# Optimization experiments

Measured on AMD Instinct MI355X. Metric: run time of the kernel, lower is better.

Reference implementation:

```python
import jax, jax.numpy as jnp
import numpy as np

NUM_NODES = 100000
NUM_EDGES = 1600000
NUM_GRAPHS = 64
D_IN = 128
HID = 256
N_ATTR = 8
D_OUT = 1


def setup_inputs() -> dict:
    key = jax.random.key(0)
    ks = jax.random.split(key, 16)
    x = jax.random.normal(ks[0], (NUM_NODES, D_IN), dtype=jnp.float32)
    edge_index = jax.random.randint(ks[1], (2, NUM_EDGES), 0, NUM_NODES, dtype=jnp.int64)
    batch = jnp.sort(jax.random.randint(ks[2], (NUM_NODES,), 0, NUM_GRAPHS, dtype=jnp.int64))
    graph_attr = jax.random.normal(ks[3], (NUM_GRAPHS, N_ATTR), dtype=jnp.float32)
    def lin(k, fi, fo):
        s = 1.0 / np.sqrt(fi)
        return jax.random.uniform(k, (fi, fo), jnp.float32, -s, s)
    # SAGEConv: lin_l (applied to aggregated neighbors, has bias) + lin_r (root, no bias)
    W1l = lin(ks[4], D_IN, HID); b1 = jnp.zeros((HID,), jnp.float32)
    W1r = lin(ks[5], D_IN, HID)
    W2l = lin(ks[6], HID, HID); b2 = jnp.zeros((HID,), jnp.float32)
    W2r = lin(ks[7], HID, HID)
    Wf1 = lin(ks[8], HID + N_ATTR, HID); bf1 = jnp.zeros((HID,), jnp.float32)
    Wf2 = lin(ks[9], HID, D_OUT); bf2 = jnp.zeros((D_OUT,), jnp.float32)
    return {"x": x, "edge_index": edge_index, "batch": batch, "graph_attr": graph_attr,
            "W1l": W1l, "b1": b1, "W1r": W1r, "W2l": W2l, "b2": b2, "W2r": W2r,
            "Wf1": Wf1, "bf1": bf1, "Wf2": Wf2, "bf2": bf2}


def _mean_agg(h, src, dst, num_segments):
    # gather source features, scatter-mean into destination nodes
    s = jax.ops.segment_sum(h[src], dst, num_segments=num_segments)
    cnt = jax.ops.segment_sum(jnp.ones((src.shape[0], 1), h.dtype), dst, num_segments=num_segments)
    return s / jnp.maximum(cnt, 1.0)


def _sage(h, src, dst, Wl, b, Wr):
    agg = _mean_agg(h, src, dst, h.shape[0])
    return agg @ Wl + b + h @ Wr


def reference(x, edge_index, batch, graph_attr, W1l, b1, W1r, W2l, b2, W2r, Wf1, bf1, Wf2, bf2):
    src, dst = edge_index[0], edge_index[1]
    h = jax.nn.relu(_sage(x, src, dst, W1l, b1, W1r))
    h = _sage(h, src, dst, W2l, b2, W2r)
    # global mean pool over graphs
    gsum = jax.ops.segment_sum(h, batch, num_segments=NUM_GRAPHS)
    gcnt = jax.ops.segment_sum(jnp.ones((h.shape[0], 1), h.dtype), batch, num_segments=NUM_GRAPHS)
    g = gsum / jnp.maximum(gcnt, 1.0)
    g = jnp.concatenate([g, graph_attr.reshape(-1, N_ATTR)], axis=1)
    g = jax.nn.relu(g @ Wf1 + bf1)
    return g @ Wf2 + bf2
```

## Files before the change

### kernel.cpp

```cpp
#include <hip/hip_runtime.h>
#include <stdint.h>

#define NN 100000
#define NE 1600000
#define NG 64
#define DIN 128
#define HID 256
#define NATTR 8
#define NBK 391
#define CAP 6144
#define PCH 4096
#define BWW 25000
#define CB 12756

typedef unsigned short u16;
typedef __attribute__((ext_vector_type(8))) short s16x8;
typedef __attribute__((ext_vector_type(4))) float f32x4;

__device__ __forceinline__ int imaxi(int a, int b) { return a > b ? a : b; }
__device__ __forceinline__ u16 f2bf(float f) {
    unsigned u = __float_as_uint(f);
    return (u16)((u + 0x7fffu + ((u >> 16) & 1u)) >> 16);
}
__device__ __forceinline__ void gload16(const void* g, void* l) {
    __builtin_amdgcn_global_load_lds((const __attribute__((address_space(1))) void*)g,
                                     (__attribute__((address_space(3))) void*)l, 16, 0, 0);
}


__global__ void k_prep(const float4* __restrict__ x4, ushort4* __restrict__ xb4,
                       const float* __restrict__ W1l, const float* __restrict__ W1r,
                       u16* __restrict__ W1lt, u16* __restrict__ W1rt,
                       float4* __restrict__ P84, const int* __restrict__ batch,
                       int* __restrict__ goff, int* __restrict__ gcnt,
                       int* __restrict__ cursor) {
    int b = blockIdx.x, t = threadIdx.x;
    if (b < CB) {
        int i = b * 256 + t;
        const int NX4 = NN * DIN / 4;
        if (i < NX4) {
            float4 v = x4[i];
            ushort4 o;
            o.x = f2bf(v.x); o.y = f2bf(v.y); o.z = f2bf(v.z); o.w = f2bf(v.w);
            xb4[i] = o;
        } else {
            int j = i - NX4;
            if (j < 32768) {
                int n = j >> 7, k = j & 127;
                W1lt[j] = f2bf(W1l[k * HID + n]);
            } else if (j < 65536) {
                int jj = j - 32768;
                int n = jj >> 7, k = jj & 127;
                W1rt[jj] = f2bf(W1r[k * HID + n]);
            }
        }
    } else if (b < CB + 256) {
        int i = (b - CB) * 256 + t;
        P84[i] = make_float4(0.f, 0.f, 0.f, 0.f);
    } else {
        for (int i = t; i < NBK; i += 256) cursor[i] = 0;
        int g = t;
        if (g <= NG) {
            int lo = 0, hi = NN;
            while (lo < hi) {
                int mid = (lo + hi) >> 1;
                if (batch[mid] < g) lo = mid + 1; else hi = mid;
            }
            goff[g] = lo;
        }
        __syncthreads();
        if (g < NG) gcnt[g] = goff[g + 1] - goff[g];
    }
}


__global__ __launch_bounds__(256) void k_part(const int* __restrict__ ei,
                                              int* __restrict__ cursor,
                                              unsigned* __restrict__ pairs) {
    __shared__ unsigned spk[PCH];
    __shared__ unsigned short sbk[PCH];
    __shared__ int hist[NBK], gb[NBK];
    __shared__ int sc[512];
    int t = threadIdx.x;
    int c0 = blockIdx.x * PCH;
    int n = NE - c0; if (n > PCH) n = PCH;
    for (int i = t; i < NBK; i += 256) hist[i] = 0;
    __syncthreads();
    unsigned mypk[16]; unsigned short mybk[16]; int myoff[16];
#pragma unroll
    for (int j = 0; j < 16; j++) {
        int i = t + j * 256;
        myoff[j] = -1;
        if (i < n) {
            int e = c0 + i;
            unsigned d = (unsigned)__builtin_nontemporal_load(&ei[NE + e]);
            unsigned s = (unsigned)__builtin_nontemporal_load(&ei[e]);
            unsigned bk = d >> 8;
            mypk[j] = ((d & 255u) << 24) | s;
            mybk[j] = (unsigned short)bk;
            myoff[j] = atomicAdd(&hist[bk], 1);
        }
    }
    __syncthreads();
    sc[t] = (t < NBK) ? hist[t] : 0;
    sc[t + 256] = (t + 256 < NBK) ? hist[t + 256] : 0;
    __syncthreads();
    for (int off = 1; off < 512; off <<= 1) {
        int v0 = (t >= off) ? sc[t - off] : 0;
        int v1 = (t + 256 >= off) ? sc[t + 256 - off] : 0;
        __syncthreads();
        sc[t] += v0; sc[t + 256] += v1;
        __syncthreads();
    }
    if (t < NBK && hist[t] > 0) gb[t] = atomicAdd(&cursor[t], hist[t]);
    if (t + 256 < NBK && hist[t + 256] > 0)
        gb[t + 256] = atomicAdd(&cursor[t + 256], hist[t + 256]);
    __syncthreads();
#pragma unroll
    for (int j = 0; j < 16; j++) {
        if (myoff[j] >= 0) {
            int bk = mybk[j];
            int pos = sc[bk] - hist[bk] + myoff[j];
            spk[pos] = mypk[j];
            sbk[pos] = (unsigned short)bk;
        }
    }
    __syncthreads();
    for (int i = t; i < n; i += 256) {
        int bk = sbk[i];
        int local = gb[bk] + (i - (sc[bk] - hist[bk]));
        pairs[(size_t)bk * CAP + local] = spk[i];
    }
}


__global__ __launch_bounds__(256) void k_csr(const unsigned* __restrict__ pairs,
                                             const int* __restrict__ cursor,
                                             int* __restrict__ rowptr,
                                             unsigned* __restrict__ col) {
    __shared__ unsigned colL[CAP];
    __shared__ int csc[512];
    __shared__ int cnt[256], cur[256], sc[256];
    int b = blockIdx.x, t = threadIdx.x;
    csc[t] = (t < NBK) ? cursor[t] : 0;
    csc[t + 256] = (t + 256 < NBK) ? cursor[t + 256] : 0;
    __syncthreads();
    for (int off = 1; off < 512; off <<= 1) {
        int v0 = (t >= off) ? csc[t - off] : 0;
        int v1 = (t + 256 >= off) ? csc[t + 256 - off] : 0;
        __syncthreads();
        csc[t] += v0; csc[t + 256] += v1;
        __syncthreads();
    }
    int obase = (b == 0) ? 0 : csc[b - 1];
    int ecnt = cursor[b];
    const unsigned* pp = pairs + (size_t)b * CAP;
    cnt[t] = 0;
    __syncthreads();
    for (int i = t; i < ecnt; i += 256)
        atomicAdd(&cnt[pp[i] >> 24], 1);
    __syncthreads();
    sc[t] = cnt[t];
    __syncthreads();
    for (int off = 1; off < 256; off <<= 1) {
        int v = (t >= off) ? sc[t - off] : 0;
        __syncthreads();
        sc[t] += v;
        __syncthreads();
    }
    int lr = sc[t] - cnt[t];
    cur[t] = lr;
    int node = (b << 8) + t;
    if (node < NN) rowptr[node] = obase + lr;
    if (b == NBK - 1 && t == 0) rowptr[NN] = obase + ecnt;
    __syncthreads();
    for (int i = t; i < ecnt; i += 256) {
        unsigned p = pp[i];
        int dl = p >> 24;
        int pos = atomicAdd(&cur[dl], 1);
        int dd = cnt[dl]; if (dd > 32767) dd = 32767;
        colL[pos] = ((unsigned)dd << 17) | (p & 0xFFFFFFu);
    }
    __syncthreads();
    for (int i = t; i < ecnt; i += 256)
        col[obase + i] = colL[i];
}


__global__ void k_agg(const uint4* __restrict__ xb4, uint4* __restrict__ agg4,
                      const int* __restrict__ rowptr, const unsigned* __restrict__ col) {
    int node = blockIdx.x * 4 + (threadIdx.x >> 6);
    int lane = threadIdx.x & 63;
    if (node >= NN) return;
    int qtr = lane >> 4, li = lane & 15;
    int s = rowptr[node], e = rowptr[node + 1];
    float a0 = 0, a1 = 0, a2 = 0, a3 = 0, a4 = 0, a5 = 0, a6 = 0, a7 = 0;
#define ACC8(V) do { \
        a0 += __uint_as_float((V).x << 16); a1 += __uint_as_float((V).x & 0xffff0000u); \
        a2 += __uint_as_float((V).y << 16); a3 += __uint_as_float((V).y & 0xffff0000u); \
        a4 += __uint_as_float((V).z << 16); a5 += __uint_as_float((V).z & 0xffff0000u); \
        a6 += __uint_as_float((V).w << 16); a7 += __uint_as_float((V).w & 0xffff0000u); } while (0)
    int i = s;
    for (; i + 16 <= e; i += 16) {
        unsigned c0 = col[i + qtr] & 0x1FFFFu;
        unsigned c1 = col[i + 4 + qtr] & 0x1FFFFu;
        unsigned c2 = col[i + 8 + qtr] & 0x1FFFFu;
        unsigned c3 = col[i + 12 + qtr] & 0x1FFFFu;
        uint4 w0 = xb4[(size_t)c0 * 16 + li];
        uint4 w1 = xb4[(size_t)c1 * 16 + li];
        uint4 w2 = xb4[(size_t)c2 * 16 + li];
        uint4 w3 = xb4[(size_t)c3 * 16 + li];
        ACC8(w0); ACC8(w1); ACC8(w2); ACC8(w3);
    }
    for (; i + 4 <= e; i += 4) {
        unsigned c = col[i + qtr] & 0x1FFFFu;
        uint4 wv = xb4[(size_t)c * 16 + li];
        ACC8(wv);
    }
    if (i + qtr < e) {
        unsigned c = col[i + qtr] & 0x1FFFFu;
        uint4 wv = xb4[(size_t)c * 16 + li];
        ACC8(wv);
    }
#undef ACC8
    a0 += __shfl_xor(a0, 16); a1 += __shfl_xor(a1, 16);
    a2 += __shfl_xor(a2, 16); a3 += __shfl_xor(a3, 16);
    a4 += __shfl_xor(a4, 16); a5 += __shfl_xor(a5, 16);
    a6 += __shfl_xor(a6, 16); a7 += __shfl_xor(a7, 16);
    a0 += __shfl_xor(a0, 32); a1 += __shfl_xor(a1, 32);
    a2 += __shfl_xor(a2, 32); a3 += __shfl_xor(a3, 32);
    a4 += __shfl_xor(a4, 32); a5 += __shfl_xor(a5, 32);
    a6 += __shfl_xor(a6, 32); a7 += __shfl_xor(a7, 32);
    if (qtr == 0) {
        float inv = 1.f / (float)imaxi(e - s, 1);
        uint4 o;
        o.x = (((unsigned)f2bf(a1 * inv)) << 16) | (unsigned)f2bf(a0 * inv);
        o.y = (((unsigned)f2bf(a3 * inv)) << 16) | (unsigned)f2bf(a2 * inv);
        o.z = (((unsigned)f2bf(a5 * inv)) << 16) | (unsigned)f2bf(a4 * inv);
        o.w = (((unsigned)f2bf(a7 * inv)) << 16) | (unsigned)f2bf(a6 * inv);
        agg4[(size_t)node * 16 + li] = o;
    }
}


__global__ __launch_bounds__(512) void k_gemm1(
    const u16* __restrict__ agg1, const u16* __restrict__ xb,
    const u16* __restrict__ W1lt, const u16* __restrict__ W1rt,
    const float* __restrict__ b1, u16* __restrict__ h1t) {
    __shared__ u16 As[128][32];
    __shared__ u16 Bs[256][32];
    int t = threadIdx.x;
    int m0 = blockIdx.x * 128;
    int wave = t >> 6, lane = t & 63;
    int wm = wave & 1, wn = wave >> 1;
    int lm = lane & 15, quad = lane >> 4;
    int ar = t >> 2, aq = t & 3;
    f32x4 acc[4][4] = {};
    const u16* Ap = agg1;
    const u16* Bp = W1lt;
#pragma unroll
    for (int ph = 0; ph < 2; ph++) {
        for (int k0 = 0; k0 < DIN; k0 += 32) {
            gload16(Ap + (size_t)(m0 + ar) * DIN + k0 + aq * 8, &As[wave * 16][0]);
#pragma unroll
            for (int i = 0; i < 2; i++) {
                int r = (t + i * 512) >> 2;
                gload16(Bp + (size_t)r * DIN + k0 + aq * 8, &Bs[wave * 16 + i * 128][0]);
            }
            __syncthreads();
            s16x8 af[4], bfr[4];
#pragma unroll
            for (int i = 0; i < 4; i++) {
                af[i]  = *(const s16x8*)&As[wm * 64 + i * 16 + lm][quad * 8];
                bfr[i] = *(const s16x8*)&Bs[wn * 64 + i * 16 + lm][quad * 8];
            }
#pragma unroll
            for (int mi = 0; mi < 4; mi++)
#pragma unroll
                for (int ni = 0; ni < 4; ni++)
                    acc[mi][ni] = __builtin_amdgcn_mfma_f32_16x16x32_bf16(
                        af[mi], bfr[ni], acc[mi][ni], 0, 0, 0);
            __syncthreads();
        }
        Ap = xb; Bp = W1rt;
    }
#pragma unroll
    for (int ni = 0; ni < 4; ni++) {
        int colf = wn * 64 + ni * 16 + lm;
        float bias = b1[colf];
#pragma unroll
        for (int mi = 0; mi < 4; mi++) {
            int row = m0 + wm * 64 + mi * 16 + quad * 4;
            if (row < NN) {
                ushort4 o;
                o.x = f2bf(fmaxf(acc[mi][ni][0] + bias, 0.f));
                o.y = f2bf(fmaxf(acc[mi][ni][1] + bias, 0.f));
                o.z = f2bf(fmaxf(acc[mi][ni][2] + bias, 0.f));
                o.w = f2bf(fmaxf(acc[mi][ni][3] + bias, 0.f));
                *(ushort4*)(h1t + (size_t)colf * NN + row) = o;
            }
        }
    }
}


__global__ __launch_bounds__(256) void k_bw(
    const int* __restrict__ rowptr, const unsigned* __restrict__ col,
    const int* __restrict__ goff, u16* __restrict__ Wbt) {
    int b = blockIdx.x, t = threadIdx.x;
    if (b < 256) {
        __shared__ float bins[BWW];
        int g = b >> 2, w = b & 3;
        int lo = w * BWW;
        for (int i = t; i < BWW; i += 256) bins[i] = 0.f;
        __syncthreads();
        int ebeg = rowptr[goff[g]], eend = rowptr[goff[g + 1]];
        for (int i = ebeg + t; i < eend; i += 256) {
            unsigned c = col[i];
            unsigned sl = (c & 0x1FFFFu) - lo;
            if (sl < (unsigned)BWW) atomicAdd(&bins[sl], 1.0f / (float)(c >> 17));
        }
        __syncthreads();
        u16* out = Wbt + (size_t)g * NN + lo;
        for (int k = t; k < BWW / 4; k += 256) {
            ushort4 o;
            o.x = f2bf(bins[4 * k + 0]); o.y = f2bf(bins[4 * k + 1]);
            o.z = f2bf(bins[4 * k + 2]); o.w = f2bf(bins[4 * k + 3]);
            *(ushort4*)(out + 4 * k) = o;
        }
    } else {
        int g = b - 256;
        int a = goff[g], bnd = goff[g + 1];
        u16* out = Wbt + (size_t)(NG + g) * NN;
        for (int k = t; k < NN / 4; k += 256) {
            int c0 = 4 * k;
            ushort4 o;
            o.x = (c0 + 0 >= a && c0 + 0 < bnd) ? 0x3F80 : 0;
            o.y = (c0 + 1 >= a && c0 + 1 < bnd) ? 0x3F80 : 0;
            o.z = (c0 + 2 >= a && c0 + 2 < bnd) ? 0x3F80 : 0;
            o.w = (c0 + 3 >= a && c0 + 3 < bnd) ? 0x3F80 : 0;
            *(ushort4*)(out + c0) = o;
        }
    }
}


#define KCHUNK 512

__global__ __launch_bounds__(512) void k_poolg(
    const u16* __restrict__ Wbt, const u16* __restrict__ h1t, float* __restrict__ P8) {
    __shared__ u16 As[128][32];
    __shared__ u16 Bs[256][32];
    int t = threadIdx.x;
    int kbase = blockIdx.x * KCHUNK;
    int krem = NN - kbase;
    int ksteps = (krem < KCHUNK ? krem : KCHUNK) >> 5;
    int wave = t >> 6, lane = t & 63;
    int wm = wave & 1, wn = wave >> 1;
    int lm = lane & 15, quad = lane >> 4;
    int ar = t >> 2, aq = t & 3;
    float* P = P8 + (size_t)(blockIdx.x & 7) * 128 * HID;
    f32x4 acc[4][4] = {};
    for (int ks = 0; ks < ksteps; ks++) {
        int k0 = kbase + ks * 32;
        gload16(Wbt + (size_t)ar * NN + k0 + aq * 8, &As[wave * 16][0]);
#pragma unroll
        for (int i = 0; i < 2; i++) {
            int r = (t + i * 512) >> 2;
            gload16(h1t + (size_t)r * NN + k0 + aq * 8, &Bs[wave * 16 + i * 128][0]);
        }
        __syncthreads();
        s16x8 af[4], bfr[4];
#pragma unroll
        for (int i = 0; i < 4; i++) {
            af[i]  = *(const s16x8*)&As[wm * 64 + i * 16 + lm][quad * 8];
            bfr[i] = *(const s16x8*)&Bs[wn * 64 + i * 16 + lm][quad * 8];
        }
#pragma unroll
        for (int mi = 0; mi < 4; mi++)
#pragma unroll
            for (int ni = 0; ni < 4; ni++)
                acc[mi][ni] = __builtin_amdgcn_mfma_f32_16x16x32_bf16(
                    af[mi], bfr[ni], acc[mi][ni], 0, 0, 0);
        __syncthreads();
    }
#pragma unroll
    for (int mi = 0; mi < 4; mi++)
#pragma unroll
        for (int ni = 0; ni < 4; ni++) {
            int gcol = wm * 64 + mi * 16 + quad * 4;
            int feat = wn * 64 + ni * 16 + lm;
#pragma unroll
            for (int r = 0; r < 4; r++)
                atomicAdd(&P[(gcol + r) * HID + feat], acc[mi][ni][r]);
        }
}


__global__ void k_head(const float* __restrict__ P8, const int* __restrict__ gcnt,
                       const float* __restrict__ gattr,
                       const float* __restrict__ W2l, const float* __restrict__ b2,
                       const float* __restrict__ W2r,
                       const float* __restrict__ Wf1, const float* __restrict__ bf1,
                       const float* __restrict__ Wf2, const float* __restrict__ bf2v,
                       float* __restrict__ out) {
    __shared__ float pa[HID], ph[HID], gv[HID + NATTR];
    __shared__ float red[256];
    int g = blockIdx.x, t = threadIdx.x;
    float sa = 0.f, sh = 0.f;
#pragma unroll
    for (int c = 0; c < 8; c++) {
        sa += P8[(size_t)c * 128 * HID + g * HID + t];
        sh += P8[(size_t)c * 128 * HID + (NG + g) * HID + t];
    }
    pa[t] = sa; ph[t] = sh;
    __syncthreads();
    float s = 0.f;
    for (int k = 0; k < HID; k++)
        s += pa[k] * W2l[k * HID + t] + ph[k] * W2r[k * HID + t];
    float invc = 1.f / (float)imaxi(gcnt[g], 1);
    gv[t] = s * invc + b2[t];
    if (t < NATTR) gv[HID + t] = gattr[g * NATTR + t];
    __syncthreads();
    float h = bf1[t];
    for (int k = 0; k < HID + NATTR; k++) h += gv[k] * Wf1[k * HID + t];
    h = fmaxf(h, 0.f);
    red[t] = h * Wf2[t];
    __syncthreads();
    for (int off = 128; off > 0; off >>= 1) {
        if (t < off) red[t] += red[t + off];
        __syncthreads();
    }
    if (t == 0) out[g] = red[0] + bf2v[0];
}


extern "C" void kernel_launch(void* const* d_in, const int* in_sizes, int n_in,
                              void* d_out, int out_size, void* d_ws, size_t ws_size,
                              hipStream_t stream) {
    (void)in_sizes; (void)n_in; (void)out_size; (void)ws_size;
    const float* x     = (const float*)d_in[0];
    const int*   ei    = (const int*)d_in[1];
    const int*   batch = (const int*)d_in[2];
    const float* gattr = (const float*)d_in[3];
    const float* W1l   = (const float*)d_in[4];
    const float* b1    = (const float*)d_in[5];
    const float* W1r   = (const float*)d_in[6];
    const float* W2l   = (const float*)d_in[7];
    const float* b2    = (const float*)d_in[8];
    const float* W2r   = (const float*)d_in[9];
    const float* Wf1   = (const float*)d_in[10];
    const float* bf1   = (const float*)d_in[11];
    const float* Wf2   = (const float*)d_in[12];
    const float* bf2v  = (const float*)d_in[13];
    float* out = (float*)d_out;

    uint8_t* w = (uint8_t*)d_ws;
    size_t off = 0;
    auto alloc = [&](size_t bytes) -> void* {
        void* p = w + off;
        off += (bytes + 255) & ~(size_t)255;
        return p;
    };
    u16*      xb     = (u16*)alloc((size_t)NN * DIN * 2);
    u16*      agg1   = (u16*)alloc((size_t)NN * DIN * 2);
    u16*      h1t    = (u16*)alloc((size_t)NN * HID * 2);
    u16*      Wbt    = (u16*)alloc((size_t)128 * NN * 2);
    u16*      W1lt   = (u16*)alloc((size_t)HID * DIN * 2);
    u16*      W1rt   = (u16*)alloc((size_t)HID * DIN * 2);
    unsigned* pairs  = (unsigned*)alloc((size_t)NBK * CAP * 4);
    int*      rowptr = (int*)alloc((size_t)(NN + 1) * 4);
    unsigned* col    = (unsigned*)alloc((size_t)NE * 4);
    int*      cursor = (int*)alloc((NBK + 1) * 4);
    int*      goff   = (int*)alloc((NG + 1) * 4);
    int*      gcnt   = (int*)alloc(NG * 4);
    float*    P8     = (float*)alloc((size_t)8 * 128 * HID * 4);

    k_prep<<<CB + 257, 256, 0, stream>>>((const float4*)x, (ushort4*)xb, W1l, W1r,
                                         W1lt, W1rt, (float4*)P8, batch, goff, gcnt,
                                         cursor);

    k_part<<<(NE + PCH - 1) / PCH, 256, 0, stream>>>(ei, cursor, pairs);
    k_csr<<<NBK, 256, 0, stream>>>(pairs, cursor, rowptr, col);

    k_agg<<<NN / 4, 256, 0, stream>>>((const uint4*)xb, (uint4*)agg1, rowptr, col);
    k_gemm1<<<(NN + 127) / 128, 512, 0, stream>>>(agg1, xb, W1lt, W1rt, b1, h1t);

    k_bw<<<320, 256, 0, stream>>>(rowptr, col, goff, Wbt);
    k_poolg<<<(NN + KCHUNK - 1) / KCHUNK, 512, 0, stream>>>(Wbt, h1t, P8);

    k_head<<<NG, 256, 0, stream>>>(P8, gcnt, gattr, W2l, b2, W2r, Wf1, bf1, Wf2, bf2v, out);
}
```

Baseline: 361.2 us.

## Stage per-block column indices in LDS and use packed float2 accumulation in aggregation

```diff
diff --git a/kernel.cpp b/kernel.cpp
--- a/kernel.cpp
+++ b/kernel.cpp
@@ -12,10 +12,13 @@
 #define PCH 4096
 #define BWW 25000
 #define CB 12756
+#define AEL 2048
 
 typedef unsigned short u16;
 typedef __attribute__((ext_vector_type(8))) short s16x8;
 typedef __attribute__((ext_vector_type(4))) float f32x4;
+typedef __attribute__((ext_vector_type(2))) float f32x2;
+typedef __attribute__((ext_vector_type(4))) unsigned u32x4;
 
 __device__ __forceinline__ int imaxi(int a, int b) { return a > b ? a : b; }
 __device__ __forceinline__ u16 f2bf(float f) {
@@ -187,42 +190,78 @@
 }
 
 
-__global__ void k_agg(const uint4* __restrict__ xb4, uint4* __restrict__ agg4,
-                      const int* __restrict__ rowptr, const unsigned* __restrict__ col) {
-    int node = blockIdx.x * 4 + (threadIdx.x >> 6);
-    int lane = threadIdx.x & 63;
-    if (node >= NN) return;
+__global__ __launch_bounds__(256) void k_agg(const uint4* __restrict__ xb4,
+                                             uint4* __restrict__ agg4,
+                                             const int* __restrict__ rowptr,
+                                             const unsigned* __restrict__ col) {
+    __shared__ unsigned scol[AEL];
+    int t = threadIdx.x;
+    int base = blockIdx.x * 4;
+    int node = base + (t >> 6);
+    int lane = t & 63;
     int qtr = lane >> 4, li = lane & 15;
     int s = rowptr[node], e = rowptr[node + 1];
-    float a0 = 0, a1 = 0, a2 = 0, a3 = 0, a4 = 0, a5 = 0, a6 = 0, a7 = 0;
+    int bs = rowptr[base], be = rowptr[base + 4];
+    int bn = be - bs;
+    bool inl = bn <= AEL;
+    if (inl)
+        for (int j = t; j < bn; j += 256) scol[j] = col[bs + j];
+    __syncthreads();
+
+    f32x2 b01 = {0.f, 0.f}, b23 = {0.f, 0.f}, b45 = {0.f, 0.f}, b67 = {0.f, 0.f};
+
 #define ACC8(V) do { \
-        a0 += __uint_as_float((V).x << 16); a1 += __uint_as_float((V).x & 0xffff0000u); \
-        a2 += __uint_as_float((V).y << 16); a3 += __uint_as_float((V).y & 0xffff0000u); \
-        a4 += __uint_as_float((V).z << 16); a5 += __uint_as_float((V).z & 0xffff0000u); \
-        a6 += __uint_as_float((V).w << 16); a7 += __uint_as_float((V).w & 0xffff0000u); } while (0)
+        f32x2 p; \
+        p[0] = __uint_as_float((V).x << 16); p[1] = __uint_as_float((V).x & 0xffff0000u); b01 += p; \
+        p[0] = __uint_as_float((V).y << 16); p[1] = __uint_as_float((V).y & 0xffff0000u); b23 += p; \
+        p[0] = __uint_as_float((V).z << 16); p[1] = __uint_as_float((V).z & 0xffff0000u); b45 += p; \
+        p[0] = __uint_as_float((V).w << 16); p[1] = __uint_as_float((V).w & 0xffff0000u); b67 += p; \
+    } while (0)
+
+#define CL(X) scol[(X) - bs]
+#define CG(X) col[X]
+#define AGG_BODY(CIDX) do { \
+        for (; i + 16 <= e; i += 16) { \
+            unsigned c0 = (CIDX(i + qtr)) & 0x1FFFFu; \
+            unsigned c1 = (CIDX(i + 4 + qtr)) & 0x1FFFFu; \
+            unsigned c2 = (CIDX(i + 8 + qtr)) & 0x1FFFFu; \
+            unsigned c3 = (CIDX(i + 12 + qtr)) & 0x1FFFFu; \
+            uint4 w0 = xb4[(size_t)c0 * 16 + li]; \
+            uint4 w1 = xb4[(size_t)c1 * 16 + li]; \
+            uint4 w2 = xb4[(size_t)c2 * 16 + li]; \
+            uint4 w3 = xb4[(size_t)c3 * 16 + li]; \
+            ACC8(w0); ACC8(w1); ACC8(w2); ACC8(w3); \
+        } \
+        if (i + 8 <= e) { \
+            unsigned c0 = (CIDX(i + qtr)) & 0x1FFFFu; \
+            unsigned c1 = (CIDX(i + 4 + qtr)) & 0x1FFFFu; \
+            uint4 w0 = xb4[(size_t)c0 * 16 + li]; \
+            uint4 w1 = xb4[(size_t)c1 * 16 + li]; \
+            ACC8(w0); ACC8(w1); \
+            i += 8; \
+        } \
+        if (i + 4 <= e) { \
+            unsigned c = (CIDX(i + qtr)) & 0x1FFFFu; \
+            uint4 wv = xb4[(size_t)c * 16 + li]; \
+            ACC8(wv); \
+            i += 4; \
+        } \
+        if (i + qtr < e) { \
+            unsigned c = (CIDX(i + qtr)) & 0x1FFFFu; \
+            uint4 wv = xb4[(size_t)c * 16 + li]; \
+            ACC8(wv); \
+        } \
+    } while (0)
+
     int i = s;
-    for (; i + 16 <= e; i += 16) {
-        unsigned c0 = col[i + qtr] & 0x1FFFFu;
-        unsigned c1 = col[i + 4 + qtr] & 0x1FFFFu;
-        unsigned c2 = col[i + 8 + qtr] & 0x1FFFFu;
-        unsigned c3 = col[i + 12 + qtr] & 0x1FFFFu;
-        uint4 w0 = xb4[(size_t)c0 * 16 + li];
-        uint4 w1 = xb4[(size_t)c1 * 16 + li];
-        uint4 w2 = xb4[(size_t)c2 * 16 + li];
-        uint4 w3 = xb4[(size_t)c3 * 16 + li];
-        ACC8(w0); ACC8(w1); ACC8(w2); ACC8(w3);
-    }
-    for (; i + 4 <= e; i += 4) {
-        unsigned c = col[i + qtr] & 0x1FFFFu;
-        uint4 wv = xb4[(size_t)c * 16 + li];
-        ACC8(wv);
-    }
-    if (i + qtr < e) {
-        unsigned c = col[i + qtr] & 0x1FFFFu;
-        uint4 wv = xb4[(size_t)c * 16 + li];
-        ACC8(wv);
-    }
+    if (inl) { AGG_BODY(CL); } else { AGG_BODY(CG); }
+#undef AGG_BODY
+#undef CL
+#undef CG
 #undef ACC8
+
+    float a0 = b01[0], a1 = b01[1], a2 = b23[0], a3 = b23[1];
+    float a4 = b45[0], a5 = b45[1], a6 = b67[0], a7 = b67[1];
     a0 += __shfl_xor(a0, 16); a1 += __shfl_xor(a1, 16);
     a2 += __shfl_xor(a2, 16); a3 += __shfl_xor(a3, 16);
     a4 += __shfl_xor(a4, 16); a5 += __shfl_xor(a5, 16);
@@ -233,12 +272,12 @@
     a6 += __shfl_xor(a6, 32); a7 += __shfl_xor(a7, 32);
     if (qtr == 0) {
         float inv = 1.f / (float)imaxi(e - s, 1);
-        uint4 o;
-        o.x = (((unsigned)f2bf(a1 * inv)) << 16) | (unsigned)f2bf(a0 * inv);
-        o.y = (((unsigned)f2bf(a3 * inv)) << 16) | (unsigned)f2bf(a2 * inv);
-        o.z = (((unsigned)f2bf(a5 * inv)) << 16) | (unsigned)f2bf(a4 * inv);
-        o.w = (((unsigned)f2bf(a7 * inv)) << 16) | (unsigned)f2bf(a6 * inv);
-        agg4[(size_t)node * 16 + li] = o;
+        u32x4 ov;
+        ov[0] = (((unsigned)f2bf(a1 * inv)) << 16) | (unsigned)f2bf(a0 * inv);
+        ov[1] = (((unsigned)f2bf(a3 * inv)) << 16) | (unsigned)f2bf(a2 * inv);
+        ov[2] = (((unsigned)f2bf(a5 * inv)) << 16) | (unsigned)f2bf(a4 * inv);
+        ov[3] = (((unsigned)f2bf(a7 * inv)) << 16) | (unsigned)f2bf(a6 * inv);
+        __builtin_nontemporal_store(ov, (u32x4*)&agg4[(size_t)node * 16 + li]);
     }
 }
 
```

After: 370.8 us. 2.6% more time.
